# Kernel tuning notes

Hardware: AMD Instinct MI355X
Metric: run time of the kernel (lower is better)

The kernel has to match this reference:

```python
import jax, jax.numpy as jnp
import numpy as np

# Sizes
N, T, P, D = 1000, 4, 10, 13          # nodes, point types, edge types (T*(T+1)/2), basis dim per point
F, H, EA, K, E = 128, 128, 16, 64, 20000  # node feat, edge hidden, edge attr/feat, edge op bottleneck, edges
I_NODE = D * (D + 1) // 2             # 91: symmetric ('ij=ji') self-block irreps dim
I_EDGE = D * D                        # 169: generic ('ij') block irreps dim
AVG_NEIGH = 20.0


def setup_inputs() -> dict:
    ks = jax.random.split(jax.random.key(0), 16)
    Fin = H + 2 * F                   # edge-op input: [edge_msg, node_h_i, node_h_j]
    return {
        'node_feats': jax.random.normal(ks[0], (N, F), jnp.float32),
        'node_attrs': jax.random.uniform(ks[1], (N, T), dtype=jnp.float32),
        'edge_feats': jax.random.normal(ks[2], (E, EA), jnp.float32),
        'edge_attrs': jax.random.normal(ks[3], (E, EA), jnp.float32),
        'edge_index': jax.random.randint(ks[4], (2, E), 0, N),
        'node_types': jax.random.randint(ks[5], (N,), 0, T),
        'edge_types': jax.random.randint(ks[6], (E,), 0, P),
        'W_msg': jax.random.normal(ks[7], (F, F), jnp.float32) / np.float32(np.sqrt(F)),
        'W_attr': jax.random.normal(ks[8], (T, F), jnp.float32) / np.float32(np.sqrt(T)),
        'W_em': jax.random.normal(ks[9], (2 * F + 2 * EA, H), jnp.float32) / np.float32(np.sqrt(2 * F + 2 * EA)),
        'W_proj': jax.random.normal(ks[10], (Fin, K), jnp.float32) / np.float32(np.sqrt(Fin)),
        'W_node': jax.random.normal(ks[11], (T, F, I_NODE), jnp.float32) / np.float32(np.sqrt(F)),
        'W_edge': jax.random.normal(ks[12], (P, K, I_EDGE), jnp.float32) / np.float32(np.sqrt(K)),
        'cob_node': jax.random.normal(ks[13], (T, I_NODE, D, D), jnp.float32) / np.float32(D),
        'cob_edge': jax.random.normal(ks[14], (P, I_EDGE, D, D), jnp.float32) / np.float32(D),
    }


def reference(node_feats, node_attrs, edge_feats, edge_attrs, edge_index, node_types,
              edge_types, W_msg, W_attr, W_em, W_proj, W_node, W_edge, cob_node, cob_edge):
    src, dst = edge_index[0], edge_index[1]
    # --- node message passing (NodeMessageBlock, simplified linear-aggregate form) ---
    m = node_feats @ W_msg                                             # [N, F]
    agg = jax.ops.segment_sum(m[src], dst, num_segments=N) \
        + jax.ops.segment_sum(m[dst], src, num_segments=N)             # symmetric edge list: both dirs
    node_h = node_feats + agg / AVG_NEIGH + node_attrs @ W_attr        # [N, F]
    # --- edge messages (EdgeMessageBlock, simplified) ---
    e_in = jnp.concatenate([node_h[src], node_h[dst], edge_feats, edge_attrs], axis=-1)
    edge_msg = jnp.tanh(e_in @ W_em)                                   # [E, H]
    # --- self-interaction blocks: per-type gather -> op -> einsum('ni,ixy->nxy', ., cob) ---
    node_irred = jnp.einsum('nf,nfi->ni', node_h, W_node[node_types])  # [N, I_NODE]
    node_blocks = jnp.einsum('ni,nixy->nxy', node_irred, cob_node[node_types])  # [N, D, D]
    # --- interaction blocks: per-edge-type op + change of basis, transpose-symmetrized ---
    onehot = jax.nn.one_hot(edge_types, P, dtype=node_feats.dtype)     # [E, P] type selector

    def edge_block(a, b):
        h = jnp.concatenate([edge_msg, a, b], axis=-1) @ W_proj        # [E, K]
        irr = jnp.einsum('epi,ep->ei', jnp.einsum('ek,pki->epi', h, W_edge), onehot)  # [E, I_EDGE]
        return jnp.einsum('epxy,ep->exy', jnp.einsum('ei,pixy->epxy', irr, cob_edge), onehot)  # [E, D, D]

    blk_ij = edge_block(node_h[src], node_h[dst])
    blk_ji = edge_block(node_h[dst], node_h[src])
    edge_blocks = 0.5 * (blk_ij + jnp.swapaxes(blk_ji, -1, -2))        # symm_transpose
    # --- scatter blocks into the dense symmetric block matrix ---
    off = jnp.arange(D)
    nidx = jnp.arange(N)[:, None] * D + off                            # [N, D] diagonal block rows/cols
    rs = src[:, None] * D + off                                        # [E, D]
    cs = dst[:, None] * D + off
    M = jnp.zeros((N * D, N * D), node_feats.dtype)
    M = M.at[nidx[:, :, None], nidx[:, None, :]].add(node_blocks)
    M = M.at[rs[:, :, None], cs[:, None, :]].add(edge_blocks)
    M = M.at[cs[:, :, None], rs[:, None, :]].add(jnp.swapaxes(edge_blocks, -1, -2))
    return M
```

## Files before the change

kernel.cpp:

```cpp
#include <hip/hip_runtime.h>
#include <cmath>

#define NN   1000
#define TT   4
#define PP   10
#define DD   13
#define FF   128
#define HH   128
#define EAA  16
#define KDIM 64
#define EE   20000
#define I_NODE 91
#define I_EDGE 169
#define MROW  13000
#define ROW4  3250

#define WS_EBLK  0L
#define WS_M     0L
#define WS_AGG   128000L
#define WS_NBLK  3380000L
#define WS_V1    3549000L
#define WS_V2    3677000L
#define WS_U     3805000L
#define WS_WCOMB 3933000L
#define WS_WNC   4041160L
#define WS_INT   4127688L
#define IO_CNT   0
#define IO_OFF   1000
#define IO_CUR   2001
#define IO_ADJ   3001

#define NB_CE   640
#define NB_CN   512
#define NB_MSG  1000
#define NB_FRONT (NB_CE + NB_CN + NB_MSG + 1)

__global__ __launch_bounds__(256) void k_front(
    const float* __restrict__ We, const float* __restrict__ cobE,
    const float* __restrict__ Wn, const float* __restrict__ cobN,
    const float* __restrict__ nf, const float* __restrict__ Wmsg,
    float* __restrict__ Wcomb, float* __restrict__ Wnc,
    float* __restrict__ m, float* __restrict__ agg, int* __restrict__ cnt) {
  int b = blockIdx.x, t = threadIdx.x;
  if (b < NB_CE) {
    if (t < I_EDGE) {
      int pk = b, p = pk >> 6;
      float acc = 0.f;
      const float* wrow = We + pk * I_EDGE;
      const float* crow = cobE + p * I_EDGE * I_EDGE + t;
      for (int i = 0; i < I_EDGE; ++i) acc += wrow[i] * crow[i * I_EDGE];
      Wcomb[pk * I_EDGE + t] = acc;
    }
  } else if (b < NB_CE + NB_CN) {
    if (t < I_EDGE) {
      int tf = b - NB_CE, ty = tf >> 7;
      float acc = 0.f;
      const float* wrow = Wn + tf * I_NODE;
      const float* crow = cobN + ty * I_NODE * I_EDGE + t;
      for (int i = 0; i < I_NODE; ++i) acc += wrow[i] * crow[i * I_EDGE];
      Wnc[tf * I_EDGE + t] = acc;
    }
  } else if (b < NB_CE + NB_CN + NB_MSG) {
    int n = b - (NB_CE + NB_CN);
    __shared__ float row[FF];
    if (t < FF) row[t] = nf[n * FF + t];
    __syncthreads();
    if (t < FF) {
      float acc = 0.f;
#pragma unroll 8
      for (int f = 0; f < FF; ++f) acc += row[f] * Wmsg[f * FF + t];
      m[n * FF + t] = acc;
    } else {
      agg[n * FF + (t - FF)] = 0.f;
    }
  } else {
    for (int i = t; i < NN; i += 256) cnt[i] = 0;
  }
}

__global__ __launch_bounds__(256) void k_scatter(
    const float* __restrict__ m, const int* __restrict__ src,
    const int* __restrict__ dst, float* __restrict__ agg,
    int* __restrict__ cnt) {
  int idx = blockIdx.x * 256 + threadIdx.x;
  if (idx >= EE * FF) return;
  int e = idx >> 7, j = idx & 127;
  int s = src[e], d = dst[e];
  if (j == 0) { atomicAdd(&cnt[s], 1); atomicAdd(&cnt[d], 1); }
  atomicAdd(&agg[d * FF + j], m[s * FF + j]);
  atomicAdd(&agg[s * FF + j], m[d * FF + j]);
}

__global__ __launch_bounds__(192) void k_nodes(
    const float* __restrict__ nf, const float* __restrict__ agg,
    const float* __restrict__ na, const float* __restrict__ Wattr,
    const float* __restrict__ Wem, const float* __restrict__ Wproj,
    const int* __restrict__ ntype, const float* __restrict__ Wnc,
    float* __restrict__ V1, float* __restrict__ V2, float* __restrict__ U,
    float* __restrict__ nblk, const int* __restrict__ cnt,
    int* __restrict__ off, int* __restrict__ cur) {
  int t = threadIdx.x;
  if (blockIdx.x == NN) {
    __shared__ int sc[192];
    int base = t * 6, run = 0, loc[6];
#pragma unroll
    for (int i = 0; i < 6; ++i) {
      int v = (base + i < NN) ? cnt[base + i] : 0;
      loc[i] = run; run += v;
    }
    sc[t] = run;
    __syncthreads();
    for (int dd = 1; dd < 192; dd <<= 1) {
      int v = (t >= dd) ? sc[t - dd] : 0;
      __syncthreads();
      sc[t] += v;
      __syncthreads();
    }
    int excl = (t == 0) ? 0 : sc[t - 1];
#pragma unroll
    for (int i = 0; i < 6; ++i)
      if (base + i < NN) { int o = excl + loc[i]; off[base + i] = o; cur[base + i] = o; }
    if (t == 0) off[NN] = sc[191];
    return;
  }
  int n = blockIdx.x;
  int ty = ntype[n];
  __shared__ float row[FF];
  if (t < FF) {
    float a = 0.f;
#pragma unroll
    for (int q = 0; q < TT; ++q) a += na[n * TT + q] * Wattr[q * FF + t];
    row[t] = nf[n * FF + t] + agg[n * FF + t] * (1.0f / 20.0f) + a;
  }
  __syncthreads();
  if (t < FF) {
    float v1 = 0.f, v2 = 0.f;
#pragma unroll 4
    for (int f = 0; f < FF; ++f) {
      float x = row[f];
      v1 += x * Wem[f * HH + t];
      v2 += x * Wem[(FF + f) * HH + t];
    }
    V1[n * HH + t] = v1;
    V2[n * HH + t] = v2;
    int k = t & 63, half = t >> 6;
    const float* W = Wproj + (FF + half * FF) * KDIM + k;
    float u = 0.f;
#pragma unroll 4
    for (int f = 0; f < FF; ++f) u += row[f] * W[f * KDIM];
    U[n * 128 + t] = u;
  }
  if (t < I_EDGE) {
    float acc = 0.f;
    const float* W = Wnc + ty * FF * I_EDGE + t;
#pragma unroll 4
    for (int f = 0; f < FF; ++f) acc += row[f] * W[f * I_EDGE];
    nblk[n * I_EDGE + t] = acc;
  }
}

#define EB 4
__global__ __launch_bounds__(768) void k_edge_all(
    const float* __restrict__ V1, const float* __restrict__ V2,
    const float* __restrict__ U, const float* __restrict__ ef,
    const float* __restrict__ ea, const int* __restrict__ src,
    const int* __restrict__ dst, const int* __restrict__ etype,
    const float* __restrict__ Wem, const float* __restrict__ Wproj,
    const float* __restrict__ Wcomb, float* __restrict__ eblk,
    int* __restrict__ cur, int* __restrict__ adj) {
  int t = threadIdx.x;
  int ei = threadIdx.y;
  int e = blockIdx.x * EB + ei;
  int s = src[e], d = dst[e], p = etype[e];
  __shared__ __align__(16) float efa[EB][32];
  __shared__ __align__(16) float em[EB][HH];
  __shared__ __align__(16) float hp[EB][2][KDIM];
  __shared__ __align__(16) float h[EB][2][KDIM];
  __shared__ __align__(16) float tji[EB][I_EDGE];

  if (t == 0) {
    int pos = atomicAdd(&cur[s], 1); adj[pos] = 2 * e;
    int pos2 = atomicAdd(&cur[d], 1); adj[pos2] = 2 * e + 1;
  }
  if (t < 32) efa[ei][t] = (t < 16) ? ef[e * EAA + t] : ea[e * EAA + (t - 16)];
  __syncthreads();

  if (t < HH) {
    float acc = V1[s * HH + t] + V2[d * HH + t];
#pragma unroll
    for (int c = 0; c < 32; ++c) acc += efa[ei][c] * Wem[(256 + c) * HH + t];
    em[ei][t] = tanhf(acc);
  }
  __syncthreads();

  if (t < 128) {
    int k = t & 63, half = t >> 6;
    float hm = 0.f;
    for (int f = half * 64; f < half * 64 + 64; f += 4) {
      float4 mv = *(const float4*)&em[ei][f];
      hm += mv.x * Wproj[(f + 0) * KDIM + k] + mv.y * Wproj[(f + 1) * KDIM + k]
          + mv.z * Wproj[(f + 2) * KDIM + k] + mv.w * Wproj[(f + 3) * KDIM + k];
    }
    hp[ei][half][k] = hm;
  }
  __syncthreads();
  if (t < KDIM) {
    float hm = hp[ei][0][t] + hp[ei][1][t];
    h[ei][0][t] = hm + U[s * 128 + t] + U[d * 128 + 64 + t];
    h[ei][1][t] = hm + U[d * 128 + t] + U[s * 128 + 64 + t];
  }
  __syncthreads();

  float bij = 0.f, bji = 0.f;
  if (t < I_EDGE) {
    const float* W = Wcomb + p * KDIM * I_EDGE + t;
    for (int k = 0; k < KDIM; k += 4) {
      float4 hi = *(const float4*)&h[ei][0][k];
      float4 hj = *(const float4*)&h[ei][1][k];
      float w0 = W[(k + 0) * I_EDGE], w1 = W[(k + 1) * I_EDGE];
      float w2 = W[(k + 2) * I_EDGE], w3 = W[(k + 3) * I_EDGE];
      bij += hi.x * w0 + hi.y * w1 + hi.z * w2 + hi.w * w3;
      bji += hj.x * w0 + hj.y * w1 + hj.z * w2 + hj.w * w3;
    }
    tji[ei][t] = bji;
  }
  __syncthreads();
  if (t < I_EDGE) {
    int x = t / DD, y = t % DD;
    eblk[(size_t)e * I_EDGE + t] = 0.5f * (bij + tji[ei][y * DD + x]);
  }
}

__global__ __launch_bounds__(256) void k_assemble(
    const float* __restrict__ eblk, const float* __restrict__ nblk,
    const int* __restrict__ off, const int* __restrict__ adj,
    const int* __restrict__ src, const int* __restrict__ dst,
    float* __restrict__ M) {
  int n = blockIdx.x, t = threadIdx.x;
  float4* M4 = (float4*)M;
  const float4 z = make_float4(0.f, 0.f, 0.f, 0.f);
  for (int i = t; i < DD * ROW4; i += 256) {
    int r = n * DD + i / ROW4;
    M4[(size_t)r * ROW4 + (i % ROW4)] = z;
  }
  __threadfence_block();
  __syncthreads();
  if (t < I_EDGE) {
    int x = t / DD, y = t % DD;
    size_t rb = (size_t)(n * DD + x) * MROW;
    M[rb + n * DD + y] += nblk[n * I_EDGE + t];
    int o0 = off[n], o1 = off[n + 1];
    for (int idx = o0; idx < o1; ++idx) {
      int entry = adj[idx];
      int e = entry >> 1, dir = entry & 1;
      int other = dir ? src[e] : dst[e];
      float v = dir ? eblk[(size_t)e * I_EDGE + y * DD + x]
                    : eblk[(size_t)e * I_EDGE + t];
      M[rb + other * DD + y] += v;
    }
  }
}

extern "C" void kernel_launch(void* const* d_in, const int* in_sizes, int n_in,
                              void* d_out, int out_size, void* d_ws, size_t ws_size,
                              hipStream_t stream) {
  const float* node_feats = (const float*)d_in[0];
  const float* node_attrs = (const float*)d_in[1];
  const float* edge_feats = (const float*)d_in[2];
  const float* edge_attrs = (const float*)d_in[3];
  const int*   edge_index = (const int*)d_in[4];
  const int*   node_types = (const int*)d_in[5];
  const int*   edge_types = (const int*)d_in[6];
  const float* W_msg  = (const float*)d_in[7];
  const float* W_attr = (const float*)d_in[8];
  const float* W_em   = (const float*)d_in[9];
  const float* W_proj = (const float*)d_in[10];
  const float* W_node = (const float*)d_in[11];
  const float* W_edge = (const float*)d_in[12];
  const float* cob_node = (const float*)d_in[13];
  const float* cob_edge = (const float*)d_in[14];

  float* M  = (float*)d_out;
  float* ws = (float*)d_ws;
  float* eblk  = ws + WS_EBLK;
  float* m_buf = ws + WS_M;
  float* agg   = ws + WS_AGG;
  float* nblk  = ws + WS_NBLK;
  float* V1    = ws + WS_V1;
  float* V2    = ws + WS_V2;
  float* U     = ws + WS_U;
  float* Wcomb = ws + WS_WCOMB;
  float* Wnc   = ws + WS_WNC;
  int*   iw    = (int*)(ws + WS_INT);
  int*   cnt   = iw + IO_CNT;
  int*   off   = iw + IO_OFF;
  int*   cur   = iw + IO_CUR;
  int*   adj   = iw + IO_ADJ;

  const int* src = edge_index;
  const int* dst = edge_index + EE;

  k_front   <<<NB_FRONT, 256, 0, stream>>>(W_edge, cob_edge, W_node, cob_node,
                                           node_feats, W_msg, Wcomb, Wnc,
                                           m_buf, agg, cnt);
  k_scatter <<<(EE * FF) / 256, 256, 0, stream>>>(m_buf, src, dst, agg, cnt);
  k_nodes   <<<NN + 1, 192, 0, stream>>>(node_feats, agg, node_attrs, W_attr,
                                         W_em, W_proj, node_types, Wnc,
                                         V1, V2, U, nblk, cnt, off, cur);
  k_edge_all<<<dim3(EE / EB), dim3(192, 4), 0, stream>>>(V1, V2, U, edge_feats,
                                                         edge_attrs, src, dst,
                                                         edge_types, W_em, W_proj,
                                                         Wcomb, eblk, cur, adj);
  k_assemble<<<NN, 256, 0, stream>>>(eblk, nblk, off, adj, src, dst, M);
}
```

Measured before the change: 1.093 ms.

## Assemble block rows in shared memory and write each output row once

```diff
diff --git a/kernel.cpp b/kernel.cpp
--- a/kernel.cpp
+++ b/kernel.cpp
@@ -231,32 +231,83 @@
   }
 }
 
+#define MAXS 72
 __global__ __launch_bounds__(256) void k_assemble(
     const float* __restrict__ eblk, const float* __restrict__ nblk,
     const int* __restrict__ off, const int* __restrict__ adj,
     const int* __restrict__ src, const int* __restrict__ dst,
     float* __restrict__ M) {
   int n = blockIdx.x, t = threadIdx.x;
+  __shared__ float blk[MAXS][I_EDGE];
+  __shared__ signed char map8[13008];
+  __shared__ int s_ed[MAXS];
+  __shared__ short s_other[MAXS];
+  int* map32 = (int*)map8;
+  for (int i = t; i < 3252; i += 256) map32[i] = -1;
+  int o0 = off[n], o1 = off[n + 1];
+  int nent = 1 + (o1 - o0);
+  int ns = nent < MAXS ? nent : MAXS;
+  for (int i = t; i < ns; i += 256) {
+    int ed, other;
+    if (i == 0) { ed = -1; other = n; }
+    else { ed = adj[o0 + i - 1]; int e = ed >> 1; other = (ed & 1) ? src[e] : dst[e]; }
+    s_ed[i] = ed; s_other[i] = (short)other;
+  }
+  __syncthreads();
+  for (int j = t; j < ns * DD; j += 256) {
+    int i = j / DD, c = j - i * DD;
+    map8[(int)s_other[i] * DD + c] = (signed char)i;
+  }
+  for (int j = t; j < ns * I_EDGE; j += 256) {
+    int i = j / I_EDGE, cell = j - i * I_EDGE;
+    int ed = s_ed[i];
+    float v;
+    if (ed < 0)      v = nblk[n * I_EDGE + cell];
+    else if (ed & 1) v = eblk[(size_t)(ed >> 1) * I_EDGE + (cell % DD) * DD + cell / DD];
+    else             v = eblk[(size_t)(ed >> 1) * I_EDGE + cell];
+    blk[i][cell] = v;
+  }
+  __syncthreads();
+  for (int j = t; j < ns * I_EDGE; j += 256) {
+    int i = j / I_EDGE, cell = j - i * I_EDGE;
+    int cloc = cell % DD;
+    int w = map8[(int)s_other[i] * DD + cloc];
+    if (w != i) atomicAdd(&blk[w][cell], blk[i][cell]);
+  }
+  __syncthreads();
   float4* M4 = (float4*)M;
-  const float4 z = make_float4(0.f, 0.f, 0.f, 0.f);
-  for (int i = t; i < DD * ROW4; i += 256) {
-    int r = n * DD + i / ROW4;
-    M4[(size_t)r * ROW4 + (i % ROW4)] = z;
-  }
-  __threadfence_block();
-  __syncthreads();
-  if (t < I_EDGE) {
-    int x = t / DD, y = t % DD;
-    size_t rb = (size_t)(n * DD + x) * MROW;
-    M[rb + n * DD + y] += nblk[n * I_EDGE + t];
-    int o0 = off[n], o1 = off[n + 1];
-    for (int idx = o0; idx < o1; ++idx) {
-      int entry = adj[idx];
-      int e = entry >> 1, dir = entry & 1;
-      int other = dir ? src[e] : dst[e];
-      float v = dir ? eblk[(size_t)e * I_EDGE + y * DD + x]
-                    : eblk[(size_t)e * I_EDGE + t];
-      M[rb + other * DD + y] += v;
+  for (int r = 0; r < DD; ++r) {
+    float4* rowp = M4 + (size_t)(n * DD + r) * ROW4;
+    int rb = r * DD;
+    for (int c4 = t; c4 < ROW4; c4 += 256) {
+      int mp = map32[c4];
+      float4 v = make_float4(0.f, 0.f, 0.f, 0.f);
+      if (mp != -1) {
+        int col = c4 * 4;
+        signed char m0 = (signed char)(mp & 0xff);
+        signed char m1 = (signed char)((mp >> 8) & 0xff);
+        signed char m2 = (signed char)((mp >> 16) & 0xff);
+        signed char m3 = (signed char)((mp >> 24) & 0xff);
+        if (m0 >= 0) v.x = blk[m0][rb + (col + 0) % DD];
+        if (m1 >= 0) v.y = blk[m1][rb + (col + 1) % DD];
+        if (m2 >= 0) v.z = blk[m2][rb + (col + 2) % DD];
+        if (m3 >= 0) v.w = blk[m3][rb + (col + 3) % DD];
+      }
+      rowp[c4] = v;
+    }
+  }
+  if (nent > MAXS) {
+    __threadfence_block();
+    __syncthreads();
+    if (t < I_EDGE) {
+      int x = t / DD, y = t - (t / DD) * DD;
+      for (int i = MAXS; i < nent; ++i) {
+        int ed = adj[o0 + i - 1]; int e = ed >> 1;
+        int other = (ed & 1) ? src[e] : dst[e];
+        float v = (ed & 1) ? eblk[(size_t)e * I_EDGE + y * DD + x]
+                           : eblk[(size_t)e * I_EDGE + x * DD + y];
+        M[(size_t)(n * DD + x) * MROW + other * DD + y] += v;
+      }
     }
   }
 }
```

New measurement: 954.0 us. 12.7% less time.
